# Optimization experiments

Measured on AMD Instinct MI355X. Metric: run time of the kernel, lower is better.

The kernel has to match this reference:

```python
import jax, jax.numpy as jnp
import numpy as np

B, LP, NC, D, E = 8, 1000, 64, 128, 320  # batch, protein len, compound atoms, hid dim, esm dim


def _linear_params(key, din, dout):
    k1, k2 = jax.random.split(key)
    lim = 1.0 / np.sqrt(din)
    W = jax.random.uniform(k1, (din, dout), minval=-lim, maxval=lim, dtype=jnp.float32)
    b = jax.random.uniform(k2, (dout,), minval=-lim, maxval=lim, dtype=jnp.float32)
    return W, b


def setup_inputs() -> dict:
    key = jax.random.key(0)
    ks = jax.random.split(key, 14)
    inp = {
        "protein_embedding": jax.random.normal(ks[0], (B, LP, E), dtype=jnp.float32),
        "protein_feat_x": jax.random.normal(ks[1], (B, LP, D), dtype=jnp.float32),
        "compound_feats": jax.random.normal(ks[2], (B, NC, D), dtype=jnp.float32),
    }
    layers = [("emb", E, D), ("wq", D, D), ("wk", D, D), ("wv", D, D), ("wo", D, D),
              ("jp", D, D), ("jc", D, D),
              ("c1", D, 1024), ("c2", 1024, 1024), ("c3", 1024, 256), ("c4", 256, 1)]
    for i, (name, din, dout) in enumerate(layers):
        W, b = _linear_params(ks[3 + i], din, dout)
        inp[name + "_w"] = W
        inp[name + "_b"] = b
    return inp


def reference(protein_embedding, protein_feat_x, compound_feats,
              emb_w, emb_b, wq_w, wq_b, wk_w, wk_b, wv_w, wv_b, wo_w, wo_b,
              jp_w, jp_b, jc_w, jc_b,
              c1_w, c1_b, c2_w, c2_b, c3_w, c3_b, c4_w, c4_b):
    # protein sequence embedding -> hid dim
    pe = protein_embedding @ emb_w + emb_b                      # [B, LP, D]
    # single-head cross attention: query = seq embedding, key/value = graph feats
    Q = pe @ wq_w + wq_b
    K = protein_feat_x @ wk_w + wk_b
    V = protein_feat_x @ wv_w + wv_b
    scale = jnp.sqrt(jnp.asarray(D, pe.dtype))                  # n_heads=1 -> head_dim=D
    attn = jax.nn.softmax(jnp.einsum('bqd,bkd->bqk', Q, K) / scale, axis=-1)
    protein_feats = jnp.einsum('bqk,bkd->bqd', attn, V) @ wo_w + wo_b  # [B, LP, D]

    # sigmoid bilinear joint attention over (protein residue, compound atom) pairs
    P = jax.nn.relu(protein_feats) @ jp_w + jp_b                # [B, LP, D]
    C = jax.nn.relu(compound_feats) @ jc_w + jc_b               # [B, NC, D]
    A = jax.nn.sigmoid(jnp.einsum('bid,bkd->bik', P, C))        # [B, LP, NC]
    A = A / jnp.sum(A, axis=(1, 2), keepdims=True)

    # tanh outer product (the costly 4D bikj intermediate) then weighted reduction
    cp = jnp.tanh(protein_feats[:, :, None, :] * compound_feats[:, None, :, :])  # [B, LP, NC, D]
    cp_embedding = jnp.einsum('bikd,bik->bd', cp, A)            # [B, D]

    # classifier MLP (dropout is eval-mode identity)
    h = jax.nn.relu(cp_embedding @ c1_w + c1_b)
    h = jax.nn.relu(h @ c2_w + c2_b)
    h = jax.nn.relu(h @ c3_w + c3_b)
    return h @ c4_w + c4_b                                      # [B, 1]
```

## Files before the change

kernel.cpp:

```cpp
#include <hip/hip_runtime.h>
#include <hip/hip_bf16.h>
#include <math.h>

#define LP 1000
#define NCMP 64
#define NSPLIT 3

__device__ __forceinline__ float rcp_fast(float x) { return __builtin_amdgcn_rcpf(x); }

template<bool RELU_IN, bool NO_BIAS>
__device__ __forceinline__ void gemm_body(const float* X, const float* W, const float* __restrict__ bias,
                                          float* Y, int K, int rowbase)
{
    __shared__ __align__(16) float Ws[32][128];
    __shared__ __align__(16) float Xt[32][36];
    const int t  = threadIdx.x;
    const int r0 = (t >> 5) * 4;
    const int c0 = (t & 31) * 4;
    const int xr = t >> 3, xk = (t & 7) << 2;
    const int xrow = rowbase + xr;
    float4 xv = *(const float4*)(X + (long)xrow * K + xk);
    float4 wv[4];
    #pragma unroll
    for (int u = 0; u < 4; ++u) {
        int s = t + u * 256, r = s >> 5, cb = (s & 31) << 2;
        wv[u] = *(const float4*)(W + (long)r * 128 + cb);
    }
    float acc[4][4] = {};
    for (int k0 = 0; k0 < K; k0 += 32) {
        float4 xs = xv;
        if (RELU_IN) { xs.x = fmaxf(xs.x,0.f); xs.y = fmaxf(xs.y,0.f);
                       xs.z = fmaxf(xs.z,0.f); xs.w = fmaxf(xs.w,0.f); }
        Xt[xk+0][xr] = xs.x; Xt[xk+1][xr] = xs.y; Xt[xk+2][xr] = xs.z; Xt[xk+3][xr] = xs.w;
        #pragma unroll
        for (int u = 0; u < 4; ++u) {
            int s = t + u * 256, r = s >> 5, cb = (s & 31) << 2;
            *(float4*)&Ws[r][cb] = wv[u];
        }
        __syncthreads();
        if (k0 + 32 < K) {
            xv = *(const float4*)(X + (long)xrow * K + k0 + 32 + xk);
            #pragma unroll
            for (int u = 0; u < 4; ++u) {
                int s = t + u * 256, r = s >> 5, cb = (s & 31) << 2;
                wv[u] = *(const float4*)(W + (long)(k0 + 32 + r) * 128 + cb);
            }
        }
        #pragma unroll
        for (int kk = 0; kk < 32; ++kk) {
            float4 w4 = *(const float4*)&Ws[kk][c0];
            float4 x4 = *(const float4*)&Xt[kk][r0];
            acc[0][0] = fmaf(x4.x, w4.x, acc[0][0]); acc[0][1] = fmaf(x4.x, w4.y, acc[0][1]);
            acc[0][2] = fmaf(x4.x, w4.z, acc[0][2]); acc[0][3] = fmaf(x4.x, w4.w, acc[0][3]);
            acc[1][0] = fmaf(x4.y, w4.x, acc[1][0]); acc[1][1] = fmaf(x4.y, w4.y, acc[1][1]);
            acc[1][2] = fmaf(x4.y, w4.z, acc[1][2]); acc[1][3] = fmaf(x4.y, w4.w, acc[1][3]);
            acc[2][0] = fmaf(x4.z, w4.x, acc[2][0]); acc[2][1] = fmaf(x4.z, w4.y, acc[2][1]);
            acc[2][2] = fmaf(x4.z, w4.z, acc[2][2]); acc[2][3] = fmaf(x4.z, w4.w, acc[2][3]);
            acc[3][0] = fmaf(x4.w, w4.x, acc[3][0]); acc[3][1] = fmaf(x4.w, w4.y, acc[3][1]);
            acc[3][2] = fmaf(x4.w, w4.z, acc[3][2]); acc[3][3] = fmaf(x4.w, w4.w, acc[3][3]);
        }
        __syncthreads();
    }
    float4 bv = NO_BIAS ? make_float4(0.f,0.f,0.f,0.f) : *(const float4*)(bias + c0);
    #pragma unroll
    for (int i = 0; i < 4; ++i) {
        int row = rowbase + r0 + i;
        float4 o;
        o.x = acc[i][0] + bv.x; o.y = acc[i][1] + bv.y;
        o.z = acc[i][2] + bv.z; o.w = acc[i][3] + bv.w;
        *(float4*)(Y + (long)row * 128 + c0) = o;
    }
}

__global__ __launch_bounds__(256) void pre0_k(const float* __restrict__ emb_w, const float* __restrict__ emb_b,
                                              const float* __restrict__ wq_w, const float* __restrict__ wq_b,
                                              const float* __restrict__ wv_w, const float* __restrict__ wv_b,
                                              const float* __restrict__ wo_w, const float* __restrict__ wo_b,
                                              float* __restrict__ Wp, float* __restrict__ bp,
                                              float* __restrict__ Wvo, float* __restrict__ bvo,
                                              float* __restrict__ zbase)
{
    const int bid = blockIdx.x;
    if (bid < 10) { gemm_body<false,true>(emb_w, wq_w, nullptr, Wp, 128, bid * 32); return; }
    if (bid >= 11 && bid < 15) { gemm_body<false,true>(wv_w, wo_w, nullptr, Wvo, 128, (bid - 11) * 32); return; }
    int t = threadIdx.x;
    if (bid == 10 && t >= 128) {
        for (int i = t - 128; i < 1032; i += 128) zbase[i] = 0.f;
        return;
    }
    if (t < 128) {
        const float* vb = (bid == 10) ? emb_b : wv_b;
        const float* Wm = (bid == 10) ? wq_w  : wo_w;
        const float* ab = (bid == 10) ? wq_b  : wo_b;
        float a0 = 0.f, a1 = 0.f, a2 = 0.f, a3 = 0.f;
        for (int k = 0; k < 128; k += 4) {
            a0 = fmaf(vb[k+0], Wm[(k+0)*128 + t], a0);
            a1 = fmaf(vb[k+1], Wm[(k+1)*128 + t], a1);
            a2 = fmaf(vb[k+2], Wm[(k+2)*128 + t], a2);
            a3 = fmaf(vb[k+3], Wm[(k+3)*128 + t], a3);
        }
        float* dst = (bid == 10) ? bp : bvo;
        dst[t] = (a0 + a1) + (a2 + a3) + ab[t];
    }
}

__global__ __launch_bounds__(256) void qkv_k(const float* __restrict__ PE, const float* __restrict__ Wp,
                                             const float* __restrict__ bp, const float* __restrict__ PFX,
                                             const float* __restrict__ wk_w, const float* __restrict__ wk_b,
                                             const float* __restrict__ CF, const float* __restrict__ jc_w,
                                             const float* __restrict__ jc_b,
                                             float* __restrict__ Qo, float* __restrict__ Ko, float* __restrict__ Cj)
{
    if (blockIdx.x < 250)
        gemm_body<false,false>(PE, Wp, bp, Qo, 320, blockIdx.x * 32);
    else if (blockIdx.x < 500)
        gemm_body<false,false>(PFX, wk_w, wk_b, Ko, 128, (blockIdx.x - 250) * 32);
    else
        gemm_body<true,false>(CF, jc_w, jc_b, Cj, 128, (blockIdx.x - 500) * 32);
}

__global__ __launch_bounds__(256) void flash6_k(const float* __restrict__ Q, const float* __restrict__ Kg,
                                                const float* __restrict__ Vg, float* __restrict__ Opart,
                                                float* __restrict__ mpart, float* __restrict__ lpart)
{
    __shared__ __align__(16) float Qs[48][132];
    __shared__ __align__(16) float KVs[64][132];
    __shared__ __align__(16) float Ps[48][68];
    const int t  = threadIdx.x;
    const int tr = t >> 4;
    const int tc = t & 15;
    const int qt = blockIdx.x, sp = blockIdx.y, b = blockIdx.z;
    const int q0 = qt * 48;
    const int kt0 = (sp * 16) / NSPLIT;
    const int kt1 = ((sp + 1) * 16) / NSPLIT;
    const float SCALE = 0.08838834764831845f;
    const float L2E   = 1.4426950408889634f;

    #pragma unroll
    for (int u = 0; u < 6; ++u) {
        int s = t + u * 256, r = s >> 5, cb = (s & 31) << 2;
        float4 v = make_float4(0.f, 0.f, 0.f, 0.f);
        if (q0 + r < LP) v = *(const float4*)(Q + ((long)b * LP + q0 + r) * 128 + cb);
        *(float4*)&Qs[r][cb] = v;
    }
    float m_i[3] = { -3.0e38f, -3.0e38f, -3.0e38f };
    float l_i[3] = { 0.f, 0.f, 0.f };
    float Oa[3][8] = {};

    for (int kt = kt0; kt < kt1; ++kt) {
        const int key0 = kt * 64;
        __syncthreads();
        #pragma unroll
        for (int u = 0; u < 8; ++u) {
            int s = t + u * 256, r = s >> 5, cb = (s & 31) << 2;
            float4 v = make_float4(0.f, 0.f, 0.f, 0.f);
            if (key0 + r < LP) v = *(const float4*)(Kg + ((long)b * LP + key0 + r) * 128 + cb);
            *(float4*)&KVs[r][cb] = v;
        }
        __syncthreads();
        float sacc[3][4] = {};
        #pragma unroll 4
        for (int d4 = 0; d4 < 32; ++d4) {
            float4 q0v = *(const float4*)&Qs[3 * tr + 0][d4 << 2];
            float4 q1v = *(const float4*)&Qs[3 * tr + 1][d4 << 2];
            float4 q2v = *(const float4*)&Qs[3 * tr + 2][d4 << 2];
            #pragma unroll
            for (int j = 0; j < 4; ++j) {
                float4 kv = *(const float4*)&KVs[tc + (j << 4)][d4 << 2];
                sacc[0][j] += q0v.x*kv.x + q0v.y*kv.y + q0v.z*kv.z + q0v.w*kv.w;
                sacc[1][j] += q1v.x*kv.x + q1v.y*kv.y + q1v.z*kv.z + q1v.w*kv.w;
                sacc[2][j] += q2v.x*kv.x + q2v.y*kv.y + q2v.z*kv.z + q2v.w*kv.w;
            }
        }
        __syncthreads();
        float4 vreg[8];
        #pragma unroll
        for (int u = 0; u < 8; ++u) {
            int s = t + u * 256, r = s >> 5, cb = (s & 31) << 2;
            vreg[u] = make_float4(0.f, 0.f, 0.f, 0.f);
            if (key0 + r < LP) vreg[u] = *(const float4*)(Vg + ((long)b * LP + key0 + r) * 128 + cb);
        }
        #pragma unroll
        for (int j = 0; j < 4; ++j) {
            bool valid = (key0 + tc + (j << 4)) < LP;
            #pragma unroll
            for (int i = 0; i < 3; ++i) {
                float sv = sacc[i][j] * SCALE;
                sacc[i][j] = valid ? sv : -3.0e38f;
            }
        }
        #pragma unroll
        for (int i = 0; i < 3; ++i) {
            float tm = fmaxf(fmaxf(sacc[i][0], sacc[i][1]), fmaxf(sacc[i][2], sacc[i][3]));
            tm = fmaxf(tm, __shfl_xor(tm, 1));
            tm = fmaxf(tm, __shfl_xor(tm, 2));
            tm = fmaxf(tm, __shfl_xor(tm, 4));
            tm = fmaxf(tm, __shfl_xor(tm, 8));
            float mnew  = fmaxf(m_i[i], tm);
            float alpha = exp2f((m_i[i] - mnew) * L2E);
            float ps = 0.f;
            #pragma unroll
            for (int j = 0; j < 4; ++j) {
                float p = exp2f((sacc[i][j] - mnew) * L2E);
                Ps[3 * tr + i][tc + (j << 4)] = p;
                ps += p;
            }
            ps += __shfl_xor(ps, 1);
            ps += __shfl_xor(ps, 2);
            ps += __shfl_xor(ps, 4);
            ps += __shfl_xor(ps, 8);
            l_i[i] = l_i[i] * alpha + ps;
            m_i[i] = mnew;
            #pragma unroll
            for (int j = 0; j < 8; ++j) Oa[i][j] *= alpha;
        }
        #pragma unroll
        for (int u = 0; u < 8; ++u) {
            int s = t + u * 256, r = s >> 5, cb = (s & 31) << 2;
            *(float4*)&KVs[r][cb] = vreg[u];
        }
        __syncthreads();
        #pragma unroll 2
        for (int cg = 0; cg < 16; ++cg) {
            float4 pa = *(const float4*)&Ps[3 * tr + 0][cg << 2];
            float4 pb = *(const float4*)&Ps[3 * tr + 1][cg << 2];
            float4 pc = *(const float4*)&Ps[3 * tr + 2][cg << 2];
            #pragma unroll
            for (int e = 0; e < 4; ++e) {
                int c = (cg << 2) + e;
                float4 va = *(const float4*)&KVs[c][tc << 2];
                float4 vb = *(const float4*)&KVs[c][64 + (tc << 2)];
                float p0 = (e == 0) ? pa.x : (e == 1) ? pa.y : (e == 2) ? pa.z : pa.w;
                float p1 = (e == 0) ? pb.x : (e == 1) ? pb.y : (e == 2) ? pb.z : pb.w;
                float p2 = (e == 0) ? pc.x : (e == 1) ? pc.y : (e == 2) ? pc.z : pc.w;
                Oa[0][0] = fmaf(p0, va.x, Oa[0][0]); Oa[0][1] = fmaf(p0, va.y, Oa[0][1]);
                Oa[0][2] = fmaf(p0, va.z, Oa[0][2]); Oa[0][3] = fmaf(p0, va.w, Oa[0][3]);
                Oa[0][4] = fmaf(p0, vb.x, Oa[0][4]); Oa[0][5] = fmaf(p0, vb.y, Oa[0][5]);
                Oa[0][6] = fmaf(p0, vb.z, Oa[0][6]); Oa[0][7] = fmaf(p0, vb.w, Oa[0][7]);
                Oa[1][0] = fmaf(p1, va.x, Oa[1][0]); Oa[1][1] = fmaf(p1, va.y, Oa[1][1]);
                Oa[1][2] = fmaf(p1, va.z, Oa[1][2]); Oa[1][3] = fmaf(p1, va.w, Oa[1][3]);
                Oa[1][4] = fmaf(p1, vb.x, Oa[1][4]); Oa[1][5] = fmaf(p1, vb.y, Oa[1][5]);
                Oa[1][6] = fmaf(p1, vb.z, Oa[1][6]); Oa[1][7] = fmaf(p1, vb.w, Oa[1][7]);
                Oa[2][0] = fmaf(p2, va.x, Oa[2][0]); Oa[2][1] = fmaf(p2, va.y, Oa[2][1]);
                Oa[2][2] = fmaf(p2, va.z, Oa[2][2]); Oa[2][3] = fmaf(p2, va.w, Oa[2][3]);
                Oa[2][4] = fmaf(p2, vb.x, Oa[2][4]); Oa[2][5] = fmaf(p2, vb.y, Oa[2][5]);
                Oa[2][6] = fmaf(p2, vb.z, Oa[2][6]); Oa[2][7] = fmaf(p2, vb.w, Oa[2][7]);
            }
        }
    }
    #pragma unroll
    for (int i = 0; i < 3; ++i) {
        int row = q0 + 3 * tr + i;
        if (row < LP) {
            long base = ((long)sp * 1024000) + ((long)b * LP + row) * 128;
            *(float4*)(Opart + base + (tc << 2))      = make_float4(Oa[i][0], Oa[i][1], Oa[i][2], Oa[i][3]);
            *(float4*)(Opart + base + 64 + (tc << 2)) = make_float4(Oa[i][4], Oa[i][5], Oa[i][6], Oa[i][7]);
            if (tc == 0) {
                mpart[(long)sp * 8000 + b * LP + row] = m_i[i];
                lpart[(long)sp * 8000 + b * LP + row] = l_i[i];
            }
        }
    }
}

__global__ __launch_bounds__(256) void megatail_k(
    const float* __restrict__ Opart, const float* __restrict__ mp, const float* __restrict__ lp,
    const float* __restrict__ Wvo, const float* __restrict__ bvo,
    const float* __restrict__ jp_w, const float* __restrict__ jp_b,
    const float* __restrict__ Cj, const float* __restrict__ CF,
    float* __restrict__ Asum, float* __restrict__ cpe)
{
    __shared__ __align__(16) float WsA[32][132];
    __shared__ __align__(16) float Xt[32][20];
    __shared__ __align__(16) float AttS[16][132];
    __shared__ __align__(16) float Csh[64][132];
    __shared__ __align__(16) float Ash[16][64];
    __shared__ __align__(16) float AshT[64][20];
    __shared__ float red[256];
    const int t = threadIdx.x;
    const int p0 = blockIdx.x * 16;
    const int b  = blockIdx.y;
    const float L2E = 1.4426950408889634f;

    #pragma unroll
    for (int u = 0; u < 8; ++u) {
        int s = t + u * 256, r = s >> 5, cb = (s & 31) << 2;
        *(float4*)&Csh[r][cb] = *(const float4*)(Cj + ((long)b * NCMP + r) * 128 + cb);
    }

    const int r0 = (t >> 5) * 2, c0 = (t & 31) * 4;
    const int xr = t >> 3, xk = (t & 7) << 2;
    int prow = p0 + xr; if (prow > LP - 1) prow = LP - 1;
    const long g = (long)b * LP + prow;
    float wgt[NSPLIT]; float linv = 0.f;
    if (t < 128) {
        float mm = -3.0e38f;
        #pragma unroll
        for (int s = 0; s < NSPLIT; ++s) mm = fmaxf(mm, mp[g + (long)s * 8000]);
        float ls = 0.f;
        #pragma unroll
        for (int s = 0; s < NSPLIT; ++s) {
            wgt[s] = exp2f((mp[g + (long)s * 8000] - mm) * L2E);
            ls += wgt[s] * lp[g + (long)s * 8000];
        }
        linv = 1.0f / ls;
    }
    float4 xv = make_float4(0.f,0.f,0.f,0.f);
    float4 wv[4];
    if (t < 128) {
        float4 a = make_float4(0.f,0.f,0.f,0.f);
        #pragma unroll
        for (int s = 0; s < NSPLIT; ++s) {
            float4 p = *(const float4*)(Opart + (long)s * 1024000 + g * 128 + xk);
            a.x = fmaf(wgt[s], p.x, a.x); a.y = fmaf(wgt[s], p.y, a.y);
            a.z = fmaf(wgt[s], p.z, a.z); a.w = fmaf(wgt[s], p.w, a.w);
        }
        xv = make_float4(a.x * linv, a.y * linv, a.z * linv, a.w * linv);
    }
    #pragma unroll
    for (int u = 0; u < 4; ++u) {
        int s = t + u * 256, r = s >> 5, cb = (s & 31) << 2;
        wv[u] = *(const float4*)(Wvo + (long)r * 128 + cb);
    }
    float acc[2][4] = {};
    for (int k0 = 0; k0 < 128; k0 += 32) {
        if (t < 128) { Xt[xk+0][xr]=xv.x; Xt[xk+1][xr]=xv.y; Xt[xk+2][xr]=xv.z; Xt[xk+3][xr]=xv.w; }
        #pragma unroll
        for (int u = 0; u < 4; ++u) {
            int s = t + u * 256, r = s >> 5, cb = (s & 31) << 2;
            *(float4*)&WsA[r][cb] = wv[u];
        }
        __syncthreads();
        if (k0 + 32 < 128) {
            int kn = k0 + 32;
            if (t < 128) {
                float4 a = make_float4(0.f,0.f,0.f,0.f);
                #pragma unroll
                for (int s = 0; s < NSPLIT; ++s) {
                    float4 p = *(const float4*)(Opart + (long)s * 1024000 + g * 128 + kn + xk);
                    a.x = fmaf(wgt[s], p.x, a.x); a.y = fmaf(wgt[s], p.y, a.y);
                    a.z = fmaf(wgt[s], p.z, a.z); a.w = fmaf(wgt[s], p.w, a.w);
                }
                xv = make_float4(a.x * linv, a.y * linv, a.z * linv, a.w * linv);
            }
            #pragma unroll
            for (int u = 0; u < 4; ++u) {
                int s = t + u * 256, r = s >> 5, cb = (s & 31) << 2;
                wv[u] = *(const float4*)(Wvo + (long)(kn + r) * 128 + cb);
            }
        }
        #pragma unroll
        for (int kk = 0; kk < 32; ++kk) {
            float2 x2 = *(const float2*)&Xt[kk][r0];
            float4 w4 = *(const float4*)&WsA[kk][c0];
            acc[0][0]=fmaf(x2.x,w4.x,acc[0][0]); acc[0][1]=fmaf(x2.x,w4.y,acc[0][1]);
            acc[0][2]=fmaf(x2.x,w4.z,acc[0][2]); acc[0][3]=fmaf(x2.x,w4.w,acc[0][3]);
            acc[1][0]=fmaf(x2.y,w4.x,acc[1][0]); acc[1][1]=fmaf(x2.y,w4.y,acc[1][1]);
            acc[1][2]=fmaf(x2.y,w4.z,acc[1][2]); acc[1][3]=fmaf(x2.y,w4.w,acc[1][3]);
        }
        __syncthreads();
    }
    {
        float4 bv1 = *(const float4*)(bvo + c0);
        #pragma unroll
        for (int i = 0; i < 2; ++i)
            *(float4*)&AttS[r0 + i][c0] =
                make_float4(acc[i][0]+bv1.x, acc[i][1]+bv1.y, acc[i][2]+bv1.z, acc[i][3]+bv1.w);
    }
    float4 wv2[4];
    #pragma unroll
    for (int u = 0; u < 4; ++u) {
        int s = t + u * 256, r = s >> 5, cb = (s & 31) << 2;
        wv2[u] = *(const float4*)(jp_w + (long)r * 128 + cb);
    }
    float ac2[2][4] = {};
    for (int k0 = 0; k0 < 128; k0 += 32) {
        #pragma unroll
        for (int u = 0; u < 4; ++u) {
            int s = t + u * 256, r = s >> 5, cb = (s & 31) << 2;
            *(float4*)&WsA[r][cb] = wv2[u];
        }
        __syncthreads();
        if (k0 + 32 < 128) {
            #pragma unroll
            for (int u = 0; u < 4; ++u) {
                int s = t + u * 256, r = s >> 5, cb = (s & 31) << 2;
                wv2[u] = *(const float4*)(jp_w + (long)(k0 + 32 + r) * 128 + cb);
            }
        }
        #pragma unroll
        for (int kq = 0; kq < 8; ++kq) {
            float4 xa = *(const float4*)&AttS[r0 + 0][k0 + (kq << 2)];
            float4 xb = *(const float4*)&AttS[r0 + 1][k0 + (kq << 2)];
            #pragma unroll
            for (int e = 0; e < 4; ++e) {
                float x0 = fmaxf((e==0)?xa.x:(e==1)?xa.y:(e==2)?xa.z:xa.w, 0.f);
                float x1 = fmaxf((e==0)?xb.x:(e==1)?xb.y:(e==2)?xb.z:xb.w, 0.f);
                float4 w4 = *(const float4*)&WsA[(kq << 2) + e][c0];
                ac2[0][0]=fmaf(x0,w4.x,ac2[0][0]); ac2[0][1]=fmaf(x0,w4.y,ac2[0][1]);
                ac2[0][2]=fmaf(x0,w4.z,ac2[0][2]); ac2[0][3]=fmaf(x0,w4.w,ac2[0][3]);
                ac2[1][0]=fmaf(x1,w4.x,ac2[1][0]); ac2[1][1]=fmaf(x1,w4.y,ac2[1][1]);
                ac2[1][2]=fmaf(x1,w4.z,ac2[1][2]); ac2[1][3]=fmaf(x1,w4.w,ac2[1][3]);
            }
        }
        __syncthreads();
    }
    float (*Psh)[132] = WsA;
    {
        float4 b2 = *(const float4*)(jp_b + c0);
        #pragma unroll
        for (int i = 0; i < 2; ++i)
            *(float4*)&Psh[r0 + i][c0] =
                make_float4(ac2[i][0]+b2.x, ac2[i][1]+b2.y, ac2[i][2]+b2.z, ac2[i][3]+b2.w);
    }
    __syncthreads();
    const int tr = t >> 4, tc = t & 15;
    float sacc[4] = {};
    #pragma unroll 4
    for (int d4 = 0; d4 < 32; ++d4) {
        float4 p4 = *(const float4*)&Psh[tr][d4 << 2];
        #pragma unroll
        for (int j = 0; j < 4; ++j) {
            float4 cv = *(const float4*)&Csh[tc + (j << 4)][d4 << 2];
            sacc[j] += p4.x*cv.x + p4.y*cv.y + p4.z*cv.z + p4.w*cv.w;
        }
    }
    float lsum = 0.f;
    {
        int gi = p0 + tr;
        #pragma unroll
        for (int j = 0; j < 4; ++j) {
            float sg = rcp_fast(1.f + exp2f(-sacc[j] * L2E));
            if (gi < LP) {
                Ash[tr][tc + (j << 4)]  = sg;
                AshT[tc + (j << 4)][tr] = sg;
                lsum += sg;
            }
        }
    }
    red[t] = lsum;
    __syncthreads();
    for (int off = 128; off > 0; off >>= 1) {
        if (t < off) red[t] += red[t + off];
        __syncthreads();
    }
    if (t == 0) atomicAdd(Asum + b, red[0]);
    __syncthreads();
    #pragma unroll
    for (int u = 0; u < 8; ++u) {
        int s = t + u * 256, r = s >> 5, cb = (s & 31) << 2;
        *(float4*)&Csh[r][cb] = *(const float4*)(CF + ((long)b * NCMP + r) * 128 + cb);
    }
    __syncthreads();
    const float TWO_L2E = 2.8853900817779268f;
    const int d  = t & 127;
    const int kh = t >> 7;
    const int iiN = (LP - p0 < 16) ? (LP - p0) : 16;
    float areg[16];
    #pragma unroll
    for (int ii = 0; ii < 16; ++ii) areg[ii] = AttS[ii][d] * TWO_L2E;
    float accD = 0.f;
    for (int kk = 0; kk < 32; ++kk) {
        const int k = (kh << 5) + kk;
        const float cv = Csh[k][d];
        for (int iq = 0; iq < iiN; iq += 4) {
            float4 a4 = *(const float4*)&AshT[k][iq];
            float e0 = exp2f(areg[iq+0] * cv);
            float e1 = exp2f(areg[iq+1] * cv);
            float e2 = exp2f(areg[iq+2] * cv);
            float e3 = exp2f(areg[iq+3] * cv);
            accD = fmaf(1.f - 2.f * rcp_fast(e0 + 1.f), a4.x, accD);
            accD = fmaf(1.f - 2.f * rcp_fast(e1 + 1.f), a4.y, accD);
            accD = fmaf(1.f - 2.f * rcp_fast(e2 + 1.f), a4.z, accD);
            accD = fmaf(1.f - 2.f * rcp_fast(e3 + 1.f), a4.w, accD);
        }
    }
    red[t] = accD;
    __syncthreads();
    if (t < 128) atomicAdd(cpe + (long)b * 128 + t, red[t] + red[t + 128]);
}

__global__ __launch_bounds__(256) void c12_k(const float* __restrict__ cpe, const float* __restrict__ Asum,
                                             const float* __restrict__ c1_w, const float* __restrict__ c1_b,
                                             const float* __restrict__ c2_w, float* __restrict__ part)
{
    __shared__ float sc[8][128];
    __shared__ float ins[8][8];
    const int t = threadIdx.x, ks = blockIdx.x, k0 = ks * 8;
    #pragma unroll
    for (int u = 0; u < 4; ++u) {
        int idx = t + u * 256;
        sc[idx >> 7][idx & 127] = cpe[idx] * rcp_fast(Asum[idx >> 7]);
    }
    __syncthreads();
    if (t < 64) {
        int b = t >> 3, kk = t & 7;
        int n1 = k0 + kk;
        float a0 = 0.f, a1 = 0.f, a2 = 0.f, a3 = 0.f;
        #pragma unroll 8
        for (int j = 0; j < 128; j += 4) {
            a0 = fmaf(sc[b][j+0], c1_w[(long)(j+0)*1024 + n1], a0);
            a1 = fmaf(sc[b][j+1], c1_w[(long)(j+1)*1024 + n1], a1);
            a2 = fmaf(sc[b][j+2], c1_w[(long)(j+2)*1024 + n1], a2);
            a3 = fmaf(sc[b][j+3], c1_w[(long)(j+3)*1024 + n1], a3);
        }
        ins[b][kk] = fmaxf((a0 + a1) + (a2 + a3) + c1_b[n1], 0.f);
    }
    __syncthreads();
    const int n = (t & 63) * 4 + (t >> 6) * 256;
    float4 acc[8] = {};
    #pragma unroll
    for (int kk = 0; kk < 8; ++kk) {
        float4 w4 = *(const float4*)(c2_w + (long)(k0 + kk) * 1024 + n);
        #pragma unroll
        for (int b = 0; b < 8; ++b) {
            float s = ins[b][kk];
            acc[b].x = fmaf(s, w4.x, acc[b].x); acc[b].y = fmaf(s, w4.y, acc[b].y);
            acc[b].z = fmaf(s, w4.z, acc[b].z); acc[b].w = fmaf(s, w4.w, acc[b].w);
        }
    }
    #pragma unroll
    for (int b = 0; b < 8; ++b)
        *(float4*)(part + ((long)(ks * 8 + b)) * 1024 + n) = acc[b];
}

__global__ __launch_bounds__(256) void c3m_k(const float* __restrict__ part2, const float* __restrict__ c2_b,
                                             const float* __restrict__ c3_w, const float* __restrict__ c3_b,
                                             const float* __restrict__ c4_w, const float* __restrict__ c4_b,
                                             float* __restrict__ out)
{
    __shared__ float Hs[1024];
    __shared__ float red[256];
    const int t = threadIdx.x, b = blockIdx.x;
    float4 acc4 = make_float4(0.f,0.f,0.f,0.f);
    #pragma unroll 4
    for (int ks = 0; ks < 128; ++ks) {
        float4 p = *(const float4*)(part2 + ((long)(ks * 8 + b)) * 1024 + t * 4);
        acc4.x += p.x; acc4.y += p.y; acc4.z += p.z; acc4.w += p.w;
    }
    {
        float4 bb = *(const float4*)(c2_b + t * 4);
        Hs[t*4+0] = fmaxf(acc4.x + bb.x, 0.f);
        Hs[t*4+1] = fmaxf(acc4.y + bb.y, 0.f);
        Hs[t*4+2] = fmaxf(acc4.z + bb.z, 0.f);
        Hs[t*4+3] = fmaxf(acc4.w + bb.w, 0.f);
    }
    __syncthreads();
    float a0 = 0.f, a1 = 0.f, a2 = 0.f, a3 = 0.f;
    #pragma unroll 8
    for (int k = 0; k < 1024; k += 4) {
        a0 = fmaf(Hs[k+0], c3_w[(long)(k+0)*256 + t], a0);
        a1 = fmaf(Hs[k+1], c3_w[(long)(k+1)*256 + t], a1);
        a2 = fmaf(Hs[k+2], c3_w[(long)(k+2)*256 + t], a2);
        a3 = fmaf(Hs[k+3], c3_w[(long)(k+3)*256 + t], a3);
    }
    float h3v = fmaxf((a0 + a1) + (a2 + a3) + c3_b[t], 0.f);
    red[t] = h3v * c4_w[t];
    __syncthreads();
    for (int off = 128; off > 0; off >>= 1) {
        if (t < off) red[t] += red[t + off];
        __syncthreads();
    }
    if (t == 0) out[b] = red[0] + c4_b[0];
}

extern "C" void kernel_launch(void* const* d_in, const int* in_sizes, int n_in,
                              void* d_out, int out_size, void* d_ws, size_t ws_size,
                              hipStream_t stream)
{
    const float* PE   = (const float*)d_in[0];
    const float* PFX  = (const float*)d_in[1];
    const float* CF   = (const float*)d_in[2];
    const float* emb_w = (const float*)d_in[3];  const float* emb_b = (const float*)d_in[4];
    const float* wq_w  = (const float*)d_in[5];  const float* wq_b  = (const float*)d_in[6];
    const float* wk_w  = (const float*)d_in[7];  const float* wk_b  = (const float*)d_in[8];
    const float* wv_w  = (const float*)d_in[9];  const float* wv_b  = (const float*)d_in[10];
    const float* wo_w  = (const float*)d_in[11]; const float* wo_b  = (const float*)d_in[12];
    const float* jp_w  = (const float*)d_in[13]; const float* jp_b  = (const float*)d_in[14];
    const float* jc_w  = (const float*)d_in[15]; const float* jc_b  = (const float*)d_in[16];
    const float* c1_w  = (const float*)d_in[17]; const float* c1_b  = (const float*)d_in[18];
    const float* c2_w  = (const float*)d_in[19]; const float* c2_b  = (const float*)d_in[20];
    const float* c3_w  = (const float*)d_in[21]; const float* c3_b  = (const float*)d_in[22];
    const float* c4_w  = (const float*)d_in[23]; const float* c4_b  = (const float*)d_in[24];

    float* ws     = (float*)d_ws;
    float* bufQ   = ws;
    float* bufK   = bufQ   + 1024000;
    float* bufC   = bufK   + 1024000;
    float* Opart  = bufC   + 65536;
    float* mpart  = Opart  + 3072000;
    float* lpart  = mpart  + 24000;
    float* Asum   = lpart  + 24000;
    float* cpe    = Asum   + 8;
    float* bprime = cpe    + 1024;
    float* bufWp  = bprime + 128;
    float* bufWvo = bufWp  + 40960;
    float* bufbvo = bufWvo + 16384;
    float* part2  = bufQ;

    pre0_k<<<16, 256, 0, stream>>>(emb_w, emb_b, wq_w, wq_b, wv_w, wv_b, wo_w, wo_b,
                                   bufWp, bprime, bufWvo, bufbvo, Asum);
    qkv_k<<<516, 256, 0, stream>>>(PE, bufWp, bprime, PFX, wk_w, wk_b, CF, jc_w, jc_b,
                                   bufQ, bufK, bufC);
    flash6_k<<<dim3(21, NSPLIT, 8), 256, 0, stream>>>(bufQ, bufK, PFX, Opart, mpart, lpart);
    megatail_k<<<dim3(63, 8), 256, 0, stream>>>(Opart, mpart, lpart, bufWvo, bufbvo,
                                                jp_w, jp_b, bufC, CF, Asum, cpe);
    c12_k<<<128, 256, 0, stream>>>(cpe, Asum, c1_w, c1_b, c2_w, part2);
    c3m_k<<<8, 256, 0, stream>>>(part2, c2_b, c3_w, c3_b, c4_w, c4_b, (float*)d_out);
}
```

Before: 337.9 us.

## Move cross-attention to f16 MFMA with hi/lo split-precision emulation

Rewrites the flash-attention kernel to use 16x16x32 f16 MFMA instructions instead of scalar FP32 FMAs. Q, K and V are each split into high and low f16 halves, and three MFMA products per tile are summed to approximate FP32 accuracy. The QKV projection kernel now writes these split f16 buffers directly, padded to 1024 rows, and adds blocks that store a transposed, split copy of V. The key split rises from 3 to 4 with 64-row query tiles. The 3x MFMA work and extra conversion traffic are traded for much higher matrix throughput. Padding rows in the f16 buffers are never written, so they rely on the workspace contents being finite, since they are multiplied by zero probabilities.

```diff
diff --git a/kernel.cpp b/kernel.cpp
--- a/kernel.cpp
+++ b/kernel.cpp
@@ -4,16 +4,21 @@
 
 #define LP 1000
 #define NCMP 64
-#define NSPLIT 3
+#define NSPLIT 4
+
+typedef _Float16 f16;
+typedef f16   v8h __attribute__((ext_vector_type(8)));
+typedef float v4f __attribute__((ext_vector_type(4)));
 
 __device__ __forceinline__ float rcp_fast(float x) { return __builtin_amdgcn_rcpf(x); }
-
-template<bool RELU_IN, bool NO_BIAS>
-__device__ __forceinline__ void gemm_body(const float* X, const float* W, const float* __restrict__ bias,
-                                          float* Y, int K, int rowbase)
-{
-    __shared__ __align__(16) float Ws[32][128];
-    __shared__ __align__(16) float Xt[32][36];
+__device__ __forceinline__ void fsplit(float x, f16& h, f16& l) {
+    h = (f16)x; l = (f16)(x - (float)h);
+}
+
+__device__ __forceinline__ void gemm_core(float (*Ws)[128], float (*Xt)[36],
+                                          const float* X, const float* W, const float* bias,
+                                          float* Y, int K, int rowbase, bool relu_in)
+{
     const int t  = threadIdx.x;
     const int r0 = (t >> 5) * 4;
     const int c0 = (t & 31) * 4;
@@ -29,7 +34,7 @@
     float acc[4][4] = {};
     for (int k0 = 0; k0 < K; k0 += 32) {
         float4 xs = xv;
-        if (RELU_IN) { xs.x = fmaxf(xs.x,0.f); xs.y = fmaxf(xs.y,0.f);
+        if (relu_in) { xs.x = fmaxf(xs.x,0.f); xs.y = fmaxf(xs.y,0.f);
                        xs.z = fmaxf(xs.z,0.f); xs.w = fmaxf(xs.w,0.f); }
         Xt[xk+0][xr] = xs.x; Xt[xk+1][xr] = xs.y; Xt[xk+2][xr] = xs.z; Xt[xk+3][xr] = xs.w;
         #pragma unroll
@@ -61,7 +66,7 @@
         }
         __syncthreads();
     }
-    float4 bv = NO_BIAS ? make_float4(0.f,0.f,0.f,0.f) : *(const float4*)(bias + c0);
+    float4 bv = bias ? *(const float4*)(bias + c0) : make_float4(0.f,0.f,0.f,0.f);
     #pragma unroll
     for (int i = 0; i < 4; ++i) {
         int row = rowbase + r0 + i;
@@ -69,6 +74,70 @@
         o.x = acc[i][0] + bv.x; o.y = acc[i][1] + bv.y;
         o.z = acc[i][2] + bv.z; o.w = acc[i][3] + bv.w;
         *(float4*)(Y + (long)row * 128 + c0) = o;
+    }
+}
+
+struct H4 { f16 a, b, c, d; };
+
+__device__ __forceinline__ void gemm_core16(float (*Ws)[128], float (*Xt)[36],
+                                            const float* X, const float* W, const float* bias,
+                                            f16* Yhi, f16* Ylo, int K, int rowbase)
+{
+    const int t  = threadIdx.x;
+    const int r0 = (t >> 5) * 4;
+    const int c0 = (t & 31) * 4;
+    const int xr = t >> 3, xk = (t & 7) << 2;
+    const int xrow = rowbase + xr;
+    float4 xv = *(const float4*)(X + (long)xrow * K + xk);
+    float4 wv[4];
+    #pragma unroll
+    for (int u = 0; u < 4; ++u) {
+        int s = t + u * 256, r = s >> 5, cb = (s & 31) << 2;
+        wv[u] = *(const float4*)(W + (long)r * 128 + cb);
+    }
+    float acc[4][4] = {};
+    for (int k0 = 0; k0 < K; k0 += 32) {
+        Xt[xk+0][xr] = xv.x; Xt[xk+1][xr] = xv.y; Xt[xk+2][xr] = xv.z; Xt[xk+3][xr] = xv.w;
+        #pragma unroll
+        for (int u = 0; u < 4; ++u) {
+            int s = t + u * 256, r = s >> 5, cb = (s & 31) << 2;
+            *(float4*)&Ws[r][cb] = wv[u];
+        }
+        __syncthreads();
+        if (k0 + 32 < K) {
+            xv = *(const float4*)(X + (long)xrow * K + k0 + 32 + xk);
+            #pragma unroll
+            for (int u = 0; u < 4; ++u) {
+                int s = t + u * 256, r = s >> 5, cb = (s & 31) << 2;
+                wv[u] = *(const float4*)(W + (long)(k0 + 32 + r) * 128 + cb);
+            }
+        }
+        #pragma unroll
+        for (int kk = 0; kk < 32; ++kk) {
+            float4 w4 = *(const float4*)&Ws[kk][c0];
+            float4 x4 = *(const float4*)&Xt[kk][r0];
+            acc[0][0] = fmaf(x4.x, w4.x, acc[0][0]); acc[0][1] = fmaf(x4.x, w4.y, acc[0][1]);
+            acc[0][2] = fmaf(x4.x, w4.z, acc[0][2]); acc[0][3] = fmaf(x4.x, w4.w, acc[0][3]);
+            acc[1][0] = fmaf(x4.y, w4.x, acc[1][0]); acc[1][1] = fmaf(x4.y, w4.y, acc[1][1]);
+            acc[1][2] = fmaf(x4.y, w4.z, acc[1][2]); acc[1][3] = fmaf(x4.y, w4.w, acc[1][3]);
+            acc[2][0] = fmaf(x4.z, w4.x, acc[2][0]); acc[2][1] = fmaf(x4.z, w4.y, acc[2][1]);
+            acc[2][2] = fmaf(x4.z, w4.z, acc[2][2]); acc[2][3] = fmaf(x4.z, w4.w, acc[2][3]);
+            acc[3][0] = fmaf(x4.w, w4.x, acc[3][0]); acc[3][1] = fmaf(x4.w, w4.y, acc[3][1]);
+            acc[3][2] = fmaf(x4.w, w4.z, acc[3][2]); acc[3][3] = fmaf(x4.w, w4.w, acc[3][3]);
+        }
+        __syncthreads();
+    }
+    float4 bv = *(const float4*)(bias + c0);
+    #pragma unroll
+    for (int i = 0; i < 4; ++i) {
+        int row = rowbase + r0 + i;
+        int bb = row / 1000, rr = row - bb * 1000;
+        long base = ((long)bb * 1024 + rr) * 128 + c0;
+        float o0 = acc[i][0]+bv.x, o1 = acc[i][1]+bv.y, o2 = acc[i][2]+bv.z, o3 = acc[i][3]+bv.w;
+        H4 h, l;
+        fsplit(o0, h.a, l.a); fsplit(o1, h.b, l.b); fsplit(o2, h.c, l.c); fsplit(o3, h.d, l.d);
+        *(H4*)(Yhi + base) = h;
+        *(H4*)(Ylo + base) = l;
     }
 }
 
@@ -80,9 +149,11 @@
                                               float* __restrict__ Wvo, float* __restrict__ bvo,
                                               float* __restrict__ zbase)
 {
+    __shared__ __align__(16) float Ws[32][128];
+    __shared__ __align__(16) float Xt[32][36];
     const int bid = blockIdx.x;
-    if (bid < 10) { gemm_body<false,true>(emb_w, wq_w, nullptr, Wp, 128, bid * 32); return; }
-    if (bid >= 11 && bid < 15) { gemm_body<false,true>(wv_w, wo_w, nullptr, Wvo, 128, (bid - 11) * 32); return; }
+    if (bid < 10) { gemm_core(Ws, Xt, emb_w, wq_w, nullptr, Wp, 128, bid * 32, false); return; }
+    if (bid >= 11 && bid < 15) { gemm_core(Ws, Xt, wv_w, wo_w, nullptr, Wvo, 128, (bid - 11) * 32, false); return; }
     int t = threadIdx.x;
     if (bid == 10 && t >= 128) {
         for (int i = t - 128; i < 1032; i += 128) zbase[i] = 0.f;
@@ -109,155 +180,181 @@
                                              const float* __restrict__ wk_w, const float* __restrict__ wk_b,
                                              const float* __restrict__ CF, const float* __restrict__ jc_w,
                                              const float* __restrict__ jc_b,
-                                             float* __restrict__ Qo, float* __restrict__ Ko, float* __restrict__ Cj)
-{
-    if (blockIdx.x < 250)
-        gemm_body<false,false>(PE, Wp, bp, Qo, 320, blockIdx.x * 32);
-    else if (blockIdx.x < 500)
-        gemm_body<false,false>(PFX, wk_w, wk_b, Ko, 128, (blockIdx.x - 250) * 32);
-    else
-        gemm_body<true,false>(CF, jc_w, jc_b, Cj, 128, (blockIdx.x - 500) * 32);
-}
-
-__global__ __launch_bounds__(256) void flash6_k(const float* __restrict__ Q, const float* __restrict__ Kg,
-                                                const float* __restrict__ Vg, float* __restrict__ Opart,
+                                             f16* __restrict__ Qhi, f16* __restrict__ Qlo,
+                                             f16* __restrict__ Khi, f16* __restrict__ Klo,
+                                             f16* __restrict__ Vthi, f16* __restrict__ Vtlo,
+                                             float* __restrict__ Cj)
+{
+    __shared__ __align__(16) float Ws[32][128];
+    __shared__ __align__(16) float Xt[32][36];
+    const int bid = blockIdx.x;
+    if (bid < 250) { gemm_core16(Ws, Xt, PE, Wp, bp, Qhi, Qlo, 320, bid * 32); return; }
+    if (bid < 500) { gemm_core16(Ws, Xt, PFX, wk_w, wk_b, Khi, Klo, 128, (bid - 250) * 32); return; }
+    if (bid < 516) { gemm_core(Ws, Xt, CF, jc_w, jc_b, Cj, 128, (bid - 500) * 32, true); return; }
+    const int t = threadIdx.x;
+    const int rowbase = (bid - 516) * 32;
+    const int d = t >> 1, half = t & 1;
+    #pragma unroll 4
+    for (int i = 0; i < 16; ++i) {
+        int row = rowbase + half * 16 + i;
+        int bb = row / 1000, rr = row - bb * 1000;
+        float v = PFX[(long)row * 128 + d];
+        f16 h, l; fsplit(v, h, l);
+        long o = ((long)bb * 128 + d) * 1024 + rr;
+        Vthi[o] = h; Vtlo[o] = l;
+    }
+}
+
+__global__ __launch_bounds__(256) void flash7_k(const f16* __restrict__ Qhi, const f16* __restrict__ Qlo,
+                                                const f16* __restrict__ Khi, const f16* __restrict__ Klo,
+                                                const f16* __restrict__ Vthi, const f16* __restrict__ Vtlo,
+                                                float* __restrict__ Opart,
                                                 float* __restrict__ mpart, float* __restrict__ lpart)
 {
-    __shared__ __align__(16) float Qs[48][132];
-    __shared__ __align__(16) float KVs[64][132];
-    __shared__ __align__(16) float Ps[48][68];
-    const int t  = threadIdx.x;
-    const int tr = t >> 4;
-    const int tc = t & 15;
+    __shared__ __align__(16) f16 KVhi[9216];
+    __shared__ __align__(16) f16 KVlo[9216];
+    __shared__ __align__(16) f16 Pshi[4][16 * 72];
+    __shared__ __align__(16) f16 Pslo[4][16 * 72];
+    const int t    = threadIdx.x;
+    const int wv   = t >> 6;
+    const int lane = t & 63;
+    const int quad = lane >> 4;
+    const int l4   = lane & 15;
     const int qt = blockIdx.x, sp = blockIdx.y, b = blockIdx.z;
-    const int q0 = qt * 48;
-    const int kt0 = (sp * 16) / NSPLIT;
-    const int kt1 = ((sp + 1) * 16) / NSPLIT;
+    const int q0 = qt * 64;
     const float SCALE = 0.08838834764831845f;
     const float L2E   = 1.4426950408889634f;
 
-    #pragma unroll
-    for (int u = 0; u < 6; ++u) {
-        int s = t + u * 256, r = s >> 5, cb = (s & 31) << 2;
-        float4 v = make_float4(0.f, 0.f, 0.f, 0.f);
-        if (q0 + r < LP) v = *(const float4*)(Q + ((long)b * LP + q0 + r) * 128 + cb);
-        *(float4*)&Qs[r][cb] = v;
-    }
-    float m_i[3] = { -3.0e38f, -3.0e38f, -3.0e38f };
-    float l_i[3] = { 0.f, 0.f, 0.f };
-    float Oa[3][8] = {};
-
-    for (int kt = kt0; kt < kt1; ++kt) {
+    int qrow = q0 + wv * 16 + l4; if (qrow >= LP) qrow = LP - 1;
+    const long qbase = ((long)b * 1024 + qrow) * 128;
+    v8h qh[4], ql[4];
+    #pragma unroll
+    for (int kt4 = 0; kt4 < 4; ++kt4) {
+        qh[kt4] = *(const v8h*)(Qhi + qbase + kt4 * 32 + quad * 8);
+        ql[kt4] = *(const v8h*)(Qlo + qbase + kt4 * 32 + quad * 8);
+    }
+    float m_i[4] = { -3.0e38f, -3.0e38f, -3.0e38f, -3.0e38f };
+    float l_i[4] = { 0.f, 0.f, 0.f, 0.f };
+    v4f  O[8];
+    #pragma unroll
+    for (int dt = 0; dt < 8; ++dt) O[dt] = (v4f){0.f, 0.f, 0.f, 0.f};
+
+    for (int kt = sp * 4; kt < sp * 4 + 4; ++kt) {
         const int key0 = kt * 64;
         __syncthreads();
         #pragma unroll
-        for (int u = 0; u < 8; ++u) {
-            int s = t + u * 256, r = s >> 5, cb = (s & 31) << 2;
-            float4 v = make_float4(0.f, 0.f, 0.f, 0.f);
-            if (key0 + r < LP) v = *(const float4*)(Kg + ((long)b * LP + key0 + r) * 128 + cb);
-            *(float4*)&KVs[r][cb] = v;
-        }
-        __syncthreads();
-        float sacc[3][4] = {};
-        #pragma unroll 4
-        for (int d4 = 0; d4 < 32; ++d4) {
-            float4 q0v = *(const float4*)&Qs[3 * tr + 0][d4 << 2];
-            float4 q1v = *(const float4*)&Qs[3 * tr + 1][d4 << 2];
-            float4 q2v = *(const float4*)&Qs[3 * tr + 2][d4 << 2];
-            #pragma unroll
-            for (int j = 0; j < 4; ++j) {
-                float4 kv = *(const float4*)&KVs[tc + (j << 4)][d4 << 2];
-                sacc[0][j] += q0v.x*kv.x + q0v.y*kv.y + q0v.z*kv.z + q0v.w*kv.w;
-                sacc[1][j] += q1v.x*kv.x + q1v.y*kv.y + q1v.z*kv.z + q1v.w*kv.w;
-                sacc[2][j] += q2v.x*kv.x + q2v.y*kv.y + q2v.z*kv.z + q2v.w*kv.w;
-            }
-        }
-        __syncthreads();
-        float4 vreg[8];
-        #pragma unroll
-        for (int u = 0; u < 8; ++u) {
-            int s = t + u * 256, r = s >> 5, cb = (s & 31) << 2;
-            vreg[u] = make_float4(0.f, 0.f, 0.f, 0.f);
-            if (key0 + r < LP) vreg[u] = *(const float4*)(Vg + ((long)b * LP + key0 + r) * 128 + cb);
-        }
-        #pragma unroll
-        for (int j = 0; j < 4; ++j) {
-            bool valid = (key0 + tc + (j << 4)) < LP;
-            #pragma unroll
-            for (int i = 0; i < 3; ++i) {
-                float sv = sacc[i][j] * SCALE;
-                sacc[i][j] = valid ? sv : -3.0e38f;
-            }
-        }
-        #pragma unroll
-        for (int i = 0; i < 3; ++i) {
-            float tm = fmaxf(fmaxf(sacc[i][0], sacc[i][1]), fmaxf(sacc[i][2], sacc[i][3]));
+        for (int u = 0; u < 4; ++u) {
+            int ch = t + u * 256;
+            int r = ch >> 4, co = (ch & 15) * 8;
+            long ga = ((long)b * 1024 + key0 + r) * 128 + co;
+            *(v8h*)(KVhi + r * 136 + co) = *(const v8h*)(Khi + ga);
+            *(v8h*)(KVlo + r * 136 + co) = *(const v8h*)(Klo + ga);
+        }
+        __syncthreads();
+        v8h vh[4], vl[4];
+        #pragma unroll
+        for (int u = 0; u < 4; ++u) {
+            int ch = t + u * 256;
+            int d = ch >> 3, co = (ch & 7) * 8;
+            long ga = ((long)b * 128 + d) * 1024 + key0 + co;
+            vh[u] = *(const v8h*)(Vthi + ga);
+            vl[u] = *(const v8h*)(Vtlo + ga);
+        }
+        v4f S[4];
+        #pragma unroll
+        for (int nt = 0; nt < 4; ++nt) S[nt] = (v4f){0.f, 0.f, 0.f, 0.f};
+        #pragma unroll
+        for (int nt = 0; nt < 4; ++nt) {
+            const int rb = (nt * 16 + l4) * 136;
+            #pragma unroll
+            for (int kt4 = 0; kt4 < 4; ++kt4) {
+                v8h bh = *(const v8h*)(KVhi + rb + kt4 * 32 + quad * 8);
+                v8h bl = *(const v8h*)(KVlo + rb + kt4 * 32 + quad * 8);
+                S[nt] = __builtin_amdgcn_mfma_f32_16x16x32_f16(qh[kt4], bh, S[nt], 0, 0, 0);
+                S[nt] = __builtin_amdgcn_mfma_f32_16x16x32_f16(qh[kt4], bl, S[nt], 0, 0, 0);
+                S[nt] = __builtin_amdgcn_mfma_f32_16x16x32_f16(ql[kt4], bh, S[nt], 0, 0, 0);
+            }
+        }
+        #pragma unroll
+        for (int nt = 0; nt < 4; ++nt) {
+            bool valid = (key0 + nt * 16 + l4) < LP;
+            #pragma unroll
+            for (int r = 0; r < 4; ++r)
+                S[nt][r] = valid ? S[nt][r] * SCALE : -3.0e38f;
+        }
+        float alpha[4];
+        #pragma unroll
+        for (int r = 0; r < 4; ++r) {
+            float tm = fmaxf(fmaxf(S[0][r], S[1][r]), fmaxf(S[2][r], S[3][r]));
             tm = fmaxf(tm, __shfl_xor(tm, 1));
             tm = fmaxf(tm, __shfl_xor(tm, 2));
             tm = fmaxf(tm, __shfl_xor(tm, 4));
             tm = fmaxf(tm, __shfl_xor(tm, 8));
-            float mnew  = fmaxf(m_i[i], tm);
-            float alpha = exp2f((m_i[i] - mnew) * L2E);
+            float mnew = fmaxf(m_i[r], tm);
+            alpha[r] = exp2f((m_i[r] - mnew) * L2E);
             float ps = 0.f;
             #pragma unroll
-            for (int j = 0; j < 4; ++j) {
-                float p = exp2f((sacc[i][j] - mnew) * L2E);
-                Ps[3 * tr + i][tc + (j << 4)] = p;
+            for (int nt = 0; nt < 4; ++nt) {
+                float p = exp2f((S[nt][r] - mnew) * L2E);
+                S[nt][r] = p;
                 ps += p;
             }
             ps += __shfl_xor(ps, 1);
             ps += __shfl_xor(ps, 2);
             ps += __shfl_xor(ps, 4);
             ps += __shfl_xor(ps, 8);
-            l_i[i] = l_i[i] * alpha + ps;
-            m_i[i] = mnew;
-            #pragma unroll
-            for (int j = 0; j < 8; ++j) Oa[i][j] *= alpha;
-        }
-        #pragma unroll
-        for (int u = 0; u < 8; ++u) {
-            int s = t + u * 256, r = s >> 5, cb = (s & 31) << 2;
-            *(float4*)&KVs[r][cb] = vreg[u];
-        }
-        __syncthreads();
-        #pragma unroll 2
-        for (int cg = 0; cg < 16; ++cg) {
-            float4 pa = *(const float4*)&Ps[3 * tr + 0][cg << 2];
-            float4 pb = *(const float4*)&Ps[3 * tr + 1][cg << 2];
-            float4 pc = *(const float4*)&Ps[3 * tr + 2][cg << 2];
-            #pragma unroll
-            for (int e = 0; e < 4; ++e) {
-                int c = (cg << 2) + e;
-                float4 va = *(const float4*)&KVs[c][tc << 2];
-                float4 vb = *(const float4*)&KVs[c][64 + (tc << 2)];
-                float p0 = (e == 0) ? pa.x : (e == 1) ? pa.y : (e == 2) ? pa.z : pa.w;
-                float p1 = (e == 0) ? pb.x : (e == 1) ? pb.y : (e == 2) ? pb.z : pb.w;
-                float p2 = (e == 0) ? pc.x : (e == 1) ? pc.y : (e == 2) ? pc.z : pc.w;
-                Oa[0][0] = fmaf(p0, va.x, Oa[0][0]); Oa[0][1] = fmaf(p0, va.y, Oa[0][1]);
-                Oa[0][2] = fmaf(p0, va.z, Oa[0][2]); Oa[0][3] = fmaf(p0, va.w, Oa[0][3]);
-                Oa[0][4] = fmaf(p0, vb.x, Oa[0][4]); Oa[0][5] = fmaf(p0, vb.y, Oa[0][5]);
-                Oa[0][6] = fmaf(p0, vb.z, Oa[0][6]); Oa[0][7] = fmaf(p0, vb.w, Oa[0][7]);
-                Oa[1][0] = fmaf(p1, va.x, Oa[1][0]); Oa[1][1] = fmaf(p1, va.y, Oa[1][1]);
-                Oa[1][2] = fmaf(p1, va.z, Oa[1][2]); Oa[1][3] = fmaf(p1, va.w, Oa[1][3]);
-                Oa[1][4] = fmaf(p1, vb.x, Oa[1][4]); Oa[1][5] = fmaf(p1, vb.y, Oa[1][5]);
-                Oa[1][6] = fmaf(p1, vb.z, Oa[1][6]); Oa[1][7] = fmaf(p1, vb.w, Oa[1][7]);
-                Oa[2][0] = fmaf(p2, va.x, Oa[2][0]); Oa[2][1] = fmaf(p2, va.y, Oa[2][1]);
-                Oa[2][2] = fmaf(p2, va.z, Oa[2][2]); Oa[2][3] = fmaf(p2, va.w, Oa[2][3]);
-                Oa[2][4] = fmaf(p2, vb.x, Oa[2][4]); Oa[2][5] = fmaf(p2, vb.y, Oa[2][5]);
-                Oa[2][6] = fmaf(p2, vb.z, Oa[2][6]); Oa[2][7] = fmaf(p2, vb.w, Oa[2][7]);
-            }
-        }
-    }
-    #pragma unroll
-    for (int i = 0; i < 3; ++i) {
-        int row = q0 + 3 * tr + i;
+            l_i[r] = l_i[r] * alpha[r] + ps;
+            m_i[r] = mnew;
+        }
+        #pragma unroll
+        for (int dt = 0; dt < 8; ++dt) {
+            O[dt][0] *= alpha[0]; O[dt][1] *= alpha[1];
+            O[dt][2] *= alpha[2]; O[dt][3] *= alpha[3];
+        }
+        __syncthreads();
+        #pragma unroll
+        for (int u = 0; u < 4; ++u) {
+            int ch = t + u * 256;
+            int d = ch >> 3, co = (ch & 7) * 8;
+            *(v8h*)(KVhi + d * 72 + co) = vh[u];
+            *(v8h*)(KVlo + d * 72 + co) = vl[u];
+        }
+        #pragma unroll
+        for (int nt = 0; nt < 4; ++nt) {
+            int col = nt * 16 + l4;
+            #pragma unroll
+            for (int r = 0; r < 4; ++r) {
+                f16 ph, pl; fsplit(S[nt][r], ph, pl);
+                Pshi[wv][(quad * 4 + r) * 72 + col] = ph;
+                Pslo[wv][(quad * 4 + r) * 72 + col] = pl;
+            }
+        }
+        __syncthreads();
+        #pragma unroll
+        for (int kc = 0; kc < 2; ++kc) {
+            v8h pah = *(const v8h*)(Pshi[wv] + l4 * 72 + kc * 32 + quad * 8);
+            v8h pal = *(const v8h*)(Pslo[wv] + l4 * 72 + kc * 32 + quad * 8);
+            #pragma unroll
+            for (int dt = 0; dt < 8; ++dt) {
+                v8h vfh = *(const v8h*)(KVhi + (dt * 16 + l4) * 72 + kc * 32 + quad * 8);
+                v8h vfl = *(const v8h*)(KVlo + (dt * 16 + l4) * 72 + kc * 32 + quad * 8);
+                O[dt] = __builtin_amdgcn_mfma_f32_16x16x32_f16(pah, vfh, O[dt], 0, 0, 0);
+                O[dt] = __builtin_amdgcn_mfma_f32_16x16x32_f16(pah, vfl, O[dt], 0, 0, 0);
+                O[dt] = __builtin_amdgcn_mfma_f32_16x16x32_f16(pal, vfh, O[dt], 0, 0, 0);
+            }
+        }
+    }
+    #pragma unroll
+    for (int r = 0; r < 4; ++r) {
+        int row = q0 + wv * 16 + quad * 4 + r;
         if (row < LP) {
-            long base = ((long)sp * 1024000) + ((long)b * LP + row) * 128;
-            *(float4*)(Opart + base + (tc << 2))      = make_float4(Oa[i][0], Oa[i][1], Oa[i][2], Oa[i][3]);
-            *(float4*)(Opart + base + 64 + (tc << 2)) = make_float4(Oa[i][4], Oa[i][5], Oa[i][6], Oa[i][7]);
-            if (tc == 0) {
-                mpart[(long)sp * 8000 + b * LP + row] = m_i[i];
-                lpart[(long)sp * 8000 + b * LP + row] = l_i[i];
+            long base = (long)sp * 1024000 + ((long)b * LP + row) * 128;
+            #pragma unroll
+            for (int dt = 0; dt < 8; ++dt)
+                Opart[base + dt * 16 + l4] = O[dt][r];
+            if (l4 == 0) {
+                mpart[(long)sp * 8000 + b * LP + row] = m_i[r];
+                lpart[(long)sp * 8000 + b * LP + row] = l_i[r];
             }
         }
     }
@@ -287,7 +384,6 @@
         int s = t + u * 256, r = s >> 5, cb = (s & 31) << 2;
         *(float4*)&Csh[r][cb] = *(const float4*)(Cj + ((long)b * NCMP + r) * 128 + cb);
     }
-
     const int r0 = (t >> 5) * 2, c0 = (t & 31) * 4;
     const int xr = t >> 3, xk = (t & 7) << 2;
     int prow = p0 + xr; if (prow > LP - 1) prow = LP - 1;
@@ -584,25 +680,30 @@
     const float* c4_w  = (const float*)d_in[23]; const float* c4_b  = (const float*)d_in[24];
 
     float* ws     = (float*)d_ws;
-    float* bufQ   = ws;
-    float* bufK   = bufQ   + 1024000;
-    float* bufC   = bufK   + 1024000;
-    float* Opart  = bufC   + 65536;
-    float* mpart  = Opart  + 3072000;
-    float* lpart  = mpart  + 24000;
-    float* Asum   = lpart  + 24000;
-    float* cpe    = Asum   + 8;
-    float* bprime = cpe    + 1024;
+    f16*  Qhi   = (f16*)ws;
+    f16*  Qlo   = (f16*)(ws + 524288);
+    f16*  Khi   = (f16*)(ws + 1048576);
+    f16*  Klo   = (f16*)(ws + 1572864);
+    f16*  Vthi  = (f16*)(ws + 2097152);
+    f16*  Vtlo  = (f16*)(ws + 2621440);
+    float* bufC   = ws + 3145728;
+    float* Opart  = bufC + 65536;
+    float* mpart  = Opart + 4096000;
+    float* lpart  = mpart + 32000;
+    float* Asum   = lpart + 32000;
+    float* cpe    = Asum + 8;
+    float* bprime = cpe + 1024;
     float* bufWp  = bprime + 128;
-    float* bufWvo = bufWp  + 40960;
+    float* bufWvo = bufWp + 40960;
     float* bufbvo = bufWvo + 16384;
-    float* part2  = bufQ;
+    float* part2  = ws;
 
     pre0_k<<<16, 256, 0, stream>>>(emb_w, emb_b, wq_w, wq_b, wv_w, wv_b, wo_w, wo_b,
                                    bufWp, bprime, bufWvo, bufbvo, Asum);
-    qkv_k<<<516, 256, 0, stream>>>(PE, bufWp, bprime, PFX, wk_w, wk_b, CF, jc_w, jc_b,
-                                   bufQ, bufK, bufC);
-    flash6_k<<<dim3(21, NSPLIT, 8), 256, 0, stream>>>(bufQ, bufK, PFX, Opart, mpart, lpart);
+    qkv_k<<<766, 256, 0, stream>>>(PE, bufWp, bprime, PFX, wk_w, wk_b, CF, jc_w, jc_b,
+                                   Qhi, Qlo, Khi, Klo, Vthi, Vtlo, bufC);
+    flash7_k<<<dim3(16, NSPLIT, 8), 256, 0, stream>>>(Qhi, Qlo, Khi, Klo, Vthi, Vtlo,
+                                                      Opart, mpart, lpart);
     megatail_k<<<dim3(63, 8), 256, 0, stream>>>(Opart, mpart, lpart, bufWvo, bufbvo,
                                                 jp_w, jp_b, bufC, CF, Asum, cpe);
     c12_k<<<128, 256, 0, stream>>>(cpe, Asum, c1_w, c1_b, c2_w, part2);
```

Result: faster. 280.3 us (-17.1%).
